# Kernel optimization log

Measured on AMD Instinct MI355X. Metric: run time of the kernel, lower is better.

Reference implementation:

```python
import jax, jax.numpy as jnp
import numpy as np

B, C, H, W = 8, 512, 64, 64
CI = 256  # inter_channels = channel_in // 2
EPS = 1e-5  # BatchNorm eps


def conv1x1(x, w, b):
    # x: (b, c, h, w), w: (o, c), b: (o,)
    return jnp.einsum('bchw,oc->bohw', x, w) + b[None, :, None, None]


def maxpool2(x):
    b, c, h, w = x.shape
    return x.reshape(b, c, h // 2, 2, w // 2, 2).max(axis=(3, 5))


def setup_inputs() -> dict:
    key = jax.random.key(0)
    ks = jax.random.split(key, 13)
    s = 1.0 / np.sqrt(C)
    si = 1.0 / np.sqrt(CI)
    return {
        'x': jax.random.normal(ks[0], (B, C, H, W), dtype=jnp.float32),
        'w_g': jax.random.normal(ks[1], (CI, C), dtype=jnp.float32) * s,
        'b_g': jax.random.normal(ks[2], (CI,), dtype=jnp.float32) * 0.01,
        'w_theta': jax.random.normal(ks[3], (CI, C), dtype=jnp.float32) * s,
        'b_theta': jax.random.normal(ks[4], (CI,), dtype=jnp.float32) * 0.01,
        'w_phi': jax.random.normal(ks[5], (CI, C), dtype=jnp.float32) * s,
        'b_phi': jax.random.normal(ks[6], (CI,), dtype=jnp.float32) * 0.01,
        'w_out': jax.random.normal(ks[7], (C, CI), dtype=jnp.float32) * si,
        'b_out': jax.random.normal(ks[8], (C,), dtype=jnp.float32) * 0.01,
        'bn_gamma': jax.random.normal(ks[9], (C,), dtype=jnp.float32) * 0.1 + 1.0,
        'bn_beta': jax.random.normal(ks[10], (C,), dtype=jnp.float32) * 0.01,
        'bn_mean': jax.random.normal(ks[11], (C,), dtype=jnp.float32) * 0.01,
        'bn_var': jax.random.uniform(ks[12], (C,), dtype=jnp.float32, minval=0.5, maxval=1.5),
    }


def reference(x, w_g, b_g, w_theta, b_theta, w_phi, b_phi,
              w_out, b_out, bn_gamma, bn_beta, bn_mean, bn_var):
    b = x.shape[0]
    # g, phi: 1x1 conv then 2x2 maxpool (sub_sample=True)
    g_x = maxpool2(conv1x1(x, w_g, b_g)).reshape(b, CI, -1)        # (b, ci, M)
    phi_x = maxpool2(conv1x1(x, w_phi, b_phi)).reshape(b, CI, -1)  # (b, ci, M)
    theta_x = conv1x1(x, w_theta, b_theta).reshape(b, CI, -1)      # (b, ci, N)
    # f[b, n, m] = theta^T @ phi  -> softmax over m -> @ g^T
    f = jnp.einsum('bcn,bcm->bnm', theta_x, phi_x)                 # (b, N, M)
    attn = jax.nn.softmax(f, axis=-1)
    y = jnp.einsum('bnm,bcm->bcn', attn, g_x).reshape(b, CI, H, W)
    # W: 1x1 conv + BatchNorm (eval mode, running stats)
    w_y = conv1x1(y, w_out, b_out)
    inv = bn_gamma / jnp.sqrt(bn_var + EPS)
    w_y = w_y * inv[None, :, None, None] + (bn_beta - bn_mean * inv)[None, :, None, None]
    return w_y + x
```

## Files before the change

kernel.cpp:

```cpp
#include <hip/hip_runtime.h>

typedef _Float16 v8h __attribute__((ext_vector_type(8)));
typedef float v4f __attribute__((ext_vector_type(4)));
#define HF _Float16

#define Bn 8
#define Cc 512
#define CI 256
#define HW 4096
#define Mp 1024

__device__ __forceinline__ void gload16(const HF* g, HF* l) {
    __builtin_amdgcn_global_load_lds((const __attribute__((address_space(1))) void*)g,
                                     (__attribute__((address_space(3))) void*)l, 16, 0, 0);
}

__global__ __launch_bounds__(256) void prep_kernel(
    const float* __restrict__ w_g, const float* __restrict__ b_g,
    const float* __restrict__ w_th, const float* __restrict__ b_th,
    const float* __restrict__ w_ph, const float* __restrict__ b_ph,
    const float* __restrict__ w_out, const float* __restrict__ b_out,
    const float* __restrict__ gamma, const float* __restrict__ beta,
    const float* __restrict__ mean, const float* __restrict__ var,
    HF* __restrict__ wall, float* __restrict__ ball,
    HF* __restrict__ wo, float* __restrict__ scale, float* __restrict__ shift)
{
    int idx = blockIdx.x * 256 + threadIdx.x;
    if (idx < 768*512) {
        int o = idx >> 9;
        float v = (o < 256) ? w_th[idx] : (o < 512) ? w_ph[idx - 256*512] : w_g[idx - 512*512];
        wall[idx] = (HF)v;
    }
    if (idx < 512*256) wo[idx] = (HF)w_out[idx];
    if (idx < 768) ball[idx] = (idx < 256) ? b_th[idx] : (idx < 512) ? b_ph[idx-256] : b_g[idx-512];
    if (idx < 512) {
        float inv = gamma[idx] * rsqrtf(var[idx] + 1e-5f);
        scale[idx] = inv;
        shift[idx] = (b_out[idx] - mean[idx]) * inv + beta[idx];
    }
}

__global__ __launch_bounds__(256) void transpose_x_kernel(const float* __restrict__ x, HF* __restrict__ xT)
{
    __shared__ float tile[64][65];
    int b = blockIdx.z;
    int c0 = blockIdx.y * 64, s0 = blockIdx.x * 64;
    int tr = threadIdx.x >> 6, ts = threadIdx.x & 63;
    #pragma unroll
    for (int i = 0; i < 16; ++i) {
        int r = tr + i*4;
        tile[r][ts] = x[((long)(b*Cc) + c0 + r)*HW + s0 + ts];
    }
    __syncthreads();
    #pragma unroll
    for (int i = 0; i < 16; ++i) {
        int r = tr + i*4;
        xT[((long)b*HW + s0 + r)*Cc + c0 + ts] = (HF)tile[ts][r];
    }
}

__global__ __launch_bounds__(256) void transpose_h_kernel(const HF* __restrict__ src, long sSrc,
                                                          HF* __restrict__ dst, long sDst,
                                                          int R, int Cn)
{
    __shared__ HF tile[64][65];
    int b = blockIdx.z;
    int r0 = blockIdx.y * 64, c0 = blockIdx.x * 64;
    const HF* S = src + (long)b * sSrc;
    HF* D = dst + (long)b * sDst;
    int tr = threadIdx.x >> 6, tc = threadIdx.x & 63;
    #pragma unroll
    for (int i = 0; i < 16; ++i) {
        int r = tr + i*4;
        tile[r][tc] = S[(long)(r0 + r)*Cn + c0 + tc];
    }
    __syncthreads();
    #pragma unroll
    for (int i = 0; i < 16; ++i) {
        int r = tr + i*4;
        D[(long)(c0 + r)*R + r0 + tc] = tile[tc][r];
    }
}

__global__ __launch_bounds__(256) void pool_kernel(const HF* __restrict__ src, long sSrc,
                                                   HF* __restrict__ dst, long sDst)
{
    long idx = (long)blockIdx.x * 256 + threadIdx.x;
    int m = idx & 1023;
    long bc = idx >> 10;
    int c = (int)(bc & 255);
    int b = (int)(bc >> 8);
    int h2 = m >> 5, w2 = m & 31;
    const HF* p = src + (long)b*sSrc + (long)c*HW + h2*128 + w2*2;
    float v = fmaxf(fmaxf((float)p[0], (float)p[1]), fmaxf((float)p[64], (float)p[65]));
    dst[(long)b*sDst + (long)c*Mp + m] = (HF)v;
}

template<int EPI>
__global__ __launch_bounds__(256) void gemm_bt_kernel(
    const HF* __restrict__ A, long sA, const HF* __restrict__ B, long sB,
    void* __restrict__ Cv, long sC, int M, int N, int K,
    const float* __restrict__ rowBias,
    const float* __restrict__ rowScale, const float* __restrict__ rowShift,
    const float* __restrict__ Xres, long sX)
{
    __shared__ HF As[128][40];
    __shared__ HF Bs[128][40];
    int b = blockIdx.z;
    int i0 = blockIdx.y * 128;
    int j0 = blockIdx.x * 128;
    const HF* Ab = A + (long)b * sA;
    const HF* Bb = B + (long)b * sB;
    int tid = threadIdx.x;
    int lane = tid & 63, w = tid >> 6;
    int wr = w >> 1, wc = w & 1;
    int lr = lane & 15, lk = (lane >> 4) * 8;

    v4f acc[4][4];
    #pragma unroll
    for (int i = 0; i < 4; ++i)
        #pragma unroll
        for (int j = 0; j < 4; ++j) { v4f z = {0.f,0.f,0.f,0.f}; acc[i][j] = z; }

    for (int k0 = 0; k0 < K; k0 += 32) {
        #pragma unroll
        for (int q = 0; q < 2; ++q) {
            int ch = tid*2 + q;
            int row = ch >> 2;
            int c8 = (ch & 3) * 8;
            const uint4* ga = (const uint4*)(Ab + (long)(i0+row)*K + k0 + c8);
            *(uint4*)(&As[row][c8]) = *ga;
            const uint4* gb = (const uint4*)(Bb + (long)(j0+row)*K + k0 + c8);
            *(uint4*)(&Bs[row][c8]) = *gb;
        }
        __syncthreads();
        v8h af[4], bfr[4];
        #pragma unroll
        for (int mf = 0; mf < 4; ++mf)
            af[mf] = *(const v8h*)(&As[wr*64 + mf*16 + lr][lk]);
        #pragma unroll
        for (int nf = 0; nf < 4; ++nf)
            bfr[nf] = *(const v8h*)(&Bs[wc*64 + nf*16 + lr][lk]);
        #pragma unroll
        for (int mf = 0; mf < 4; ++mf)
            #pragma unroll
            for (int nf = 0; nf < 4; ++nf)
                acc[mf][nf] = __builtin_amdgcn_mfma_f32_16x16x32_f16(af[mf], bfr[nf], acc[mf][nf], 0, 0, 0);
        __syncthreads();
    }

    int rbase = (lane >> 4) * 4;
    #pragma unroll
    for (int mf = 0; mf < 4; ++mf) {
        #pragma unroll
        for (int nf = 0; nf < 4; ++nf) {
            #pragma unroll
            for (int r = 0; r < 4; ++r) {
                int row = i0 + wr*64 + mf*16 + rbase + r;
                int col = j0 + wc*64 + nf*16 + lr;
                float v = acc[mf][nf][r];
                if (EPI == 0) {
                    v += rowBias[row];
                    ((HF*)Cv + (long)b*sC)[(long)row*N + col] = (HF)v;
                } else if (EPI == 1) {
                    ((HF*)Cv + (long)b*sC)[(long)row*N + col] = (HF)v;
                } else {
                    float* Cf = (float*)Cv + (long)b*sC;
                    const float* Xb = Xres + (long)b*sX;
                    long o = (long)row*N + col;
                    Cf[o] = v * rowScale[row] + rowShift[row] + Xb[o];
                }
            }
        }
    }
}

__global__ __launch_bounds__(256) void fused_attn_kernel(
    const HF* __restrict__ Tt,
    const HF* __restrict__ Pt,
    const HF* __restrict__ G,
    HF* __restrict__ Yt)
{
    __shared__ HF P_lds[2][32][256];
    __shared__ HF G_lds[2][256][32];
    __shared__ HF P_buf[4][16][32];

    int b = blockIdx.y;
    int tid = threadIdx.x;
    int lane = tid & 63, w = tid >> 6;
    int lr = lane & 15, lkg = lane >> 4;
    int nbase = blockIdx.x * 64 + w * 16;

    const HF* Tb = Tt + ((long)b*HW + nbase) * CI;
    const HF* Pb = Pt + (long)b*Mp*CI;
    const HF* Gb = G  + (long)b*CI*Mp;

    auto stage = [&](int bsel, int m0) {
        #pragma unroll
        for (int q = 0; q < 4; ++q) {
            int i = w*4 + q;
            int dp = i*512 + lane*8;
            int prow = dp >> 8;
            int pcol = (dp & 255) ^ ((prow & 7) << 3);
            gload16(Pb + (long)(m0 + prow)*CI + pcol, &P_lds[bsel][0][0] + i*512);
            int dg = i*512 + lane*8;
            int grow = dg >> 5;
            int gcol = (dg & 31) ^ ((grow & 3) << 3);
            gload16(Gb + (long)grow*Mp + m0 + gcol, &G_lds[bsel][0][0] + i*512);
        }
    };

    v8h af[8];
    #pragma unroll
    for (int kf = 0; kf < 8; ++kf)
        af[kf] = *(const v8h*)(Tb + (long)lr*CI + kf*32 + lkg*8);

    v4f acc_y[16];
    #pragma unroll
    for (int i = 0; i < 16; ++i) { v4f z = {0.f,0.f,0.f,0.f}; acc_y[i] = z; }
    float mrun[4] = {-1e30f,-1e30f,-1e30f,-1e30f};
    float lrun[4] = {0.f,0.f,0.f,0.f};

    stage(0, 0);
    __syncthreads();

    int cur = 0;
    for (int t = 0; t < 32; ++t) {
        if (t < 31) stage(cur ^ 1, (t+1)*32);

        v4f acc[2];
        #pragma unroll
        for (int nf = 0; nf < 2; ++nf) { v4f z = {0.f,0.f,0.f,0.f}; acc[nf] = z; }
        __builtin_amdgcn_s_setprio(1);
        #pragma unroll
        for (int kf = 0; kf < 8; ++kf) {
            #pragma unroll
            for (int nf = 0; nf < 2; ++nf) {
                int prow = nf*16 + lr;
                v8h bfr = *(const v8h*)(&P_lds[cur][prow][(kf*32 + lkg*8) ^ ((prow & 7) << 3)]);
                acc[nf] = __builtin_amdgcn_mfma_f32_16x16x32_f16(af[kf], bfr, acc[nf], 0, 0, 0);
            }
        }
        __builtin_amdgcn_s_setprio(0);

        #pragma unroll
        for (int r = 0; r < 4; ++r) {
            float cm = fmaxf(acc[0][r], acc[1][r]);
            #pragma unroll
            for (int d = 1; d < 16; d <<= 1) cm = fmaxf(cm, __shfl_xor(cm, d));
            float mold = mrun[r];
            float mnew = fmaxf(mold, cm);
            mrun[r] = mnew;
            if (!__all(cm <= mold)) {
                float alpha = __expf(mold - mnew);
                lrun[r] *= alpha;
                #pragma unroll
                for (int cf = 0; cf < 16; ++cf) acc_y[cf][r] *= alpha;
            }
            int row = lkg*4 + r;
            float rs = 0.f;
            #pragma unroll
            for (int nf = 0; nf < 2; ++nf) {
                float p = __expf(acc[nf][r] - mnew);
                rs += p;
                P_buf[w][row][(nf*16 + lr) ^ ((row & 3) << 3)] = (HF)p;
            }
            #pragma unroll
            for (int d = 1; d < 16; d <<= 1) rs += __shfl_xor(rs, d);
            lrun[r] += rs;
        }

        v8h ap = *(const v8h*)(&P_buf[w][lr][(lkg*8) ^ ((lr & 3) << 3)]);
        __builtin_amdgcn_s_setprio(1);
        #pragma unroll
        for (int cf = 0; cf < 16; ++cf) {
            int grow = cf*16 + lr;
            v8h bg = *(const v8h*)(&G_lds[cur][grow][(lkg*8) ^ ((grow & 3) << 3)]);
            acc_y[cf] = __builtin_amdgcn_mfma_f32_16x16x32_f16(ap, bg, acc_y[cf], 0, 0, 0);
        }
        __builtin_amdgcn_s_setprio(0);

        __syncthreads();
        cur ^= 1;
    }

    HF* Yb = Yt + ((long)b*HW + nbase) * CI;
    #pragma unroll
    for (int r = 0; r < 4; ++r) {
        float inv = 1.f / lrun[r];
        #pragma unroll
        for (int cf = 0; cf < 16; ++cf)
            Yb[(long)(lkg*4 + r)*CI + cf*16 + lr] = (HF)(acc_y[cf][r] * inv);
    }
}

extern "C" void kernel_launch(void* const* d_in, const int* in_sizes, int n_in,
                              void* d_out, int out_size, void* d_ws, size_t ws_size,
                              hipStream_t stream)
{
    const float* x     = (const float*)d_in[0];
    const float* w_g   = (const float*)d_in[1];
    const float* b_g   = (const float*)d_in[2];
    const float* w_th  = (const float*)d_in[3];
    const float* b_th  = (const float*)d_in[4];
    const float* w_ph  = (const float*)d_in[5];
    const float* b_ph  = (const float*)d_in[6];
    const float* w_out = (const float*)d_in[7];
    const float* b_out = (const float*)d_in[8];
    const float* gamma = (const float*)d_in[9];
    const float* beta  = (const float*)d_in[10];
    const float* mean  = (const float*)d_in[11];
    const float* var   = (const float*)d_in[12];
    float* out = (float*)d_out;

    char* ws = (char*)d_ws;
    size_t off = 0;
    auto alloc = [&](size_t bytes) { void* p = ws + off; off += (bytes + 255) & ~(size_t)255; return p; };
    HF*    wall  = (HF*)alloc((size_t)768*512*2);
    float* ball  = (float*)alloc(768*4);
    HF*    wo    = (HF*)alloc((size_t)512*256*2);
    float* scale = (float*)alloc(512*4);
    float* shift = (float*)alloc(512*4);
    HF*    xT    = (HF*)alloc((size_t)Bn*HW*Cc*2);
    HF*    Full  = (HF*)alloc((size_t)Bn*768*HW*2);
    HF*    Tt    = (HF*)alloc((size_t)Bn*HW*CI*2);
    HF*    Pn    = (HF*)alloc((size_t)Bn*CI*Mp*2);
    HF*    Pt    = (HF*)alloc((size_t)Bn*Mp*CI*2);
    HF*    G     = (HF*)alloc((size_t)Bn*CI*Mp*2);
    HF*    Yt    = (HF*)alloc((size_t)Bn*HW*CI*2);

    prep_kernel<<<1536, 256, 0, stream>>>(w_g,b_g,w_th,b_th,w_ph,b_ph,w_out,b_out,gamma,beta,mean,var,
                                          wall, ball, wo, scale, shift);
    transpose_x_kernel<<<dim3(64,8,Bn), 256, 0, stream>>>(x, xT);
    gemm_bt_kernel<0><<<dim3(32,6,Bn), 256, 0, stream>>>(wall, 0, xT, (long)HW*Cc, Full, (long)768*HW,
                                                         768, HW, Cc, ball, nullptr, nullptr, nullptr, 0);
    transpose_h_kernel<<<dim3(64,4,Bn), 256, 0, stream>>>(Full, (long)768*HW, Tt, (long)HW*CI, CI, HW);
    pool_kernel<<<8192, 256, 0, stream>>>(Full + (size_t)256*HW, (long)768*HW, Pn, (long)CI*Mp);
    transpose_h_kernel<<<dim3(16,4,Bn), 256, 0, stream>>>(Pn, (long)CI*Mp, Pt, (long)Mp*CI, CI, Mp);
    pool_kernel<<<8192, 256, 0, stream>>>(Full + (size_t)512*HW, (long)768*HW, G, (long)CI*Mp);
    fused_attn_kernel<<<dim3(64,Bn), 256, 0, stream>>>(Tt, Pt, G, Yt);
    gemm_bt_kernel<2><<<dim3(32,4,Bn), 256, 0, stream>>>(wo, 0, Yt, (long)HW*CI, out, (long)Cc*HW,
                                                         Cc, HW, CI, nullptr, scale, shift, x, (long)Cc*HW);
}
```

Before: 219.6 us.

## Double-buffer GEMM via direct-to-LDS loads and restructure attention LDS layouts

The projection GEMM now uses global_load_lds into double-buffered, k-group-major LDS tiles, so the next K slice loads while the current one runs MFMAs; it also raises MFMA priority. The attention kernel swaps XOR-swizzled LDS layouts for k-group-major layouts and pads P_buf. The softmax row-sum shuffle reduction moves out of the loop to the end, and the kernel gets a two-blocks-per-CU launch bound. The risks are LDS bank conflicts in the new layouts, a divergent rescale branch in place of the wave-uniform check, and register pressure from the occupancy hint.

New measurement: 235.0 us. +7.0%, slower.

```diff
diff --git a/kernel.cpp b/kernel.cpp
--- a/kernel.cpp
+++ b/kernel.cpp
@@ -1,6 +1,7 @@
 #include <hip/hip_runtime.h>
 
 typedef _Float16 v8h __attribute__((ext_vector_type(8)));
+typedef _Float16 v4h __attribute__((ext_vector_type(4)));
 typedef float v4f __attribute__((ext_vector_type(4)));
 #define HF _Float16
 
@@ -10,7 +11,7 @@
 #define HW 4096
 #define Mp 1024
 
-__device__ __forceinline__ void gload16(const HF* g, HF* l) {
+__device__ __forceinline__ void gload16(const void* g, void* l) {
     __builtin_amdgcn_global_load_lds((const __attribute__((address_space(1))) void*)g,
                                      (__attribute__((address_space(3))) void*)l, 16, 0, 0);
 }
@@ -104,8 +105,8 @@
     const float* __restrict__ rowScale, const float* __restrict__ rowShift,
     const float* __restrict__ Xres, long sX)
 {
-    __shared__ HF As[128][40];
-    __shared__ HF Bs[128][40];
+    __shared__ alignas(16) HF As[2][4096];
+    __shared__ alignas(16) HF Bs[2][4096];
     int b = blockIdx.z;
     int i0 = blockIdx.y * 128;
     int j0 = blockIdx.x * 128;
@@ -114,7 +115,17 @@
     int tid = threadIdx.x;
     int lane = tid & 63, w = tid >> 6;
     int wr = w >> 1, wc = w & 1;
-    int lr = lane & 15, lk = (lane >> 4) * 8;
+    int lr = lane & 15, lkg = lane >> 4;
+
+    auto stage = [&](int bsel, int k0) {
+        #pragma unroll
+        for (int q = 0; q < 2; ++q) {
+            int idx = q*256 + tid;
+            int kg = idx >> 7, row = idx & 127;
+            gload16(Ab + (long)(i0+row)*K + k0 + kg*8, As[bsel] + (size_t)idx*8);
+            gload16(Bb + (long)(j0+row)*K + k0 + kg*8, Bs[bsel] + (size_t)idx*8);
+        }
+    };
 
     v4f acc[4][4];
     #pragma unroll
@@ -122,31 +133,27 @@
         #pragma unroll
         for (int j = 0; j < 4; ++j) { v4f z = {0.f,0.f,0.f,0.f}; acc[i][j] = z; }
 
+    stage(0, 0);
+    __syncthreads();
+    int cur = 0;
     for (int k0 = 0; k0 < K; k0 += 32) {
-        #pragma unroll
-        for (int q = 0; q < 2; ++q) {
-            int ch = tid*2 + q;
-            int row = ch >> 2;
-            int c8 = (ch & 3) * 8;
-            const uint4* ga = (const uint4*)(Ab + (long)(i0+row)*K + k0 + c8);
-            *(uint4*)(&As[row][c8]) = *ga;
-            const uint4* gb = (const uint4*)(Bb + (long)(j0+row)*K + k0 + c8);
-            *(uint4*)(&Bs[row][c8]) = *gb;
-        }
-        __syncthreads();
+        if (k0 + 32 < K) stage(cur ^ 1, k0 + 32);
         v8h af[4], bfr[4];
         #pragma unroll
         for (int mf = 0; mf < 4; ++mf)
-            af[mf] = *(const v8h*)(&As[wr*64 + mf*16 + lr][lk]);
+            af[mf] = *(const v8h*)(As[cur] + lkg*1024 + (wr*64 + mf*16 + lr)*8);
         #pragma unroll
         for (int nf = 0; nf < 4; ++nf)
-            bfr[nf] = *(const v8h*)(&Bs[wc*64 + nf*16 + lr][lk]);
+            bfr[nf] = *(const v8h*)(Bs[cur] + lkg*1024 + (wc*64 + nf*16 + lr)*8);
+        __builtin_amdgcn_s_setprio(1);
         #pragma unroll
         for (int mf = 0; mf < 4; ++mf)
             #pragma unroll
             for (int nf = 0; nf < 4; ++nf)
                 acc[mf][nf] = __builtin_amdgcn_mfma_f32_16x16x32_f16(af[mf], bfr[nf], acc[mf][nf], 0, 0, 0);
+        __builtin_amdgcn_s_setprio(0);
         __syncthreads();
+        cur ^= 1;
     }
 
     int rbase = (lane >> 4) * 4;
@@ -161,8 +168,6 @@
                 float v = acc[mf][nf][r];
                 if (EPI == 0) {
                     v += rowBias[row];
-                    ((HF*)Cv + (long)b*sC)[(long)row*N + col] = (HF)v;
-                } else if (EPI == 1) {
                     ((HF*)Cv + (long)b*sC)[(long)row*N + col] = (HF)v;
                 } else {
                     float* Cf = (float*)Cv + (long)b*sC;
@@ -175,15 +180,15 @@
     }
 }
 
-__global__ __launch_bounds__(256) void fused_attn_kernel(
+__global__ __launch_bounds__(256, 2) void fused_attn_kernel(
     const HF* __restrict__ Tt,
     const HF* __restrict__ Pt,
     const HF* __restrict__ G,
     HF* __restrict__ Yt)
 {
-    __shared__ HF P_lds[2][32][256];
-    __shared__ HF G_lds[2][256][32];
-    __shared__ HF P_buf[4][16][32];
+    __shared__ alignas(16) HF P_lds[2][8192];
+    __shared__ alignas(16) HF G_lds[2][8192];
+    __shared__ alignas(16) HF P_buf[4][16][36];
 
     int b = blockIdx.y;
     int tid = threadIdx.x;
@@ -198,15 +203,11 @@
     auto stage = [&](int bsel, int m0) {
         #pragma unroll
         for (int q = 0; q < 4; ++q) {
-            int i = w*4 + q;
-            int dp = i*512 + lane*8;
-            int prow = dp >> 8;
-            int pcol = (dp & 255) ^ ((prow & 7) << 3);
-            gload16(Pb + (long)(m0 + prow)*CI + pcol, &P_lds[bsel][0][0] + i*512);
-            int dg = i*512 + lane*8;
-            int grow = dg >> 5;
-            int gcol = (dg & 31) ^ ((grow & 3) << 3);
-            gload16(Gb + (long)grow*Mp + m0 + gcol, &G_lds[bsel][0][0] + i*512);
+            int idxp = (w*4 + q)*64 + lane;
+            int pkg = idxp >> 5, prow = idxp & 31;
+            gload16(Pb + (long)(m0 + prow)*CI + pkg*8, P_lds[bsel] + (size_t)idxp*8);
+            int grow = q*64 + lane;
+            gload16(Gb + (long)grow*Mp + m0 + w*8, G_lds[bsel] + ((size_t)w*256 + grow)*8);
         }
     };
 
@@ -219,7 +220,7 @@
     #pragma unroll
     for (int i = 0; i < 16; ++i) { v4f z = {0.f,0.f,0.f,0.f}; acc_y[i] = z; }
     float mrun[4] = {-1e30f,-1e30f,-1e30f,-1e30f};
-    float lrun[4] = {0.f,0.f,0.f,0.f};
+    float lsum[4] = {0.f,0.f,0.f,0.f};
 
     stage(0, 0);
     __syncthreads();
@@ -236,8 +237,7 @@
         for (int kf = 0; kf < 8; ++kf) {
             #pragma unroll
             for (int nf = 0; nf < 2; ++nf) {
-                int prow = nf*16 + lr;
-                v8h bfr = *(const v8h*)(&P_lds[cur][prow][(kf*32 + lkg*8) ^ ((prow & 7) << 3)]);
+                v8h bfr = *(const v8h*)(P_lds[cur] + (kf*4 + lkg)*256 + (nf*16 + lr)*8);
                 acc[nf] = __builtin_amdgcn_mfma_f32_16x16x32_f16(af[kf], bfr, acc[nf], 0, 0, 0);
             }
         }
@@ -248,34 +248,29 @@
             float cm = fmaxf(acc[0][r], acc[1][r]);
             #pragma unroll
             for (int d = 1; d < 16; d <<= 1) cm = fmaxf(cm, __shfl_xor(cm, d));
-            float mold = mrun[r];
-            float mnew = fmaxf(mold, cm);
-            mrun[r] = mnew;
-            if (!__all(cm <= mold)) {
-                float alpha = __expf(mold - mnew);
-                lrun[r] *= alpha;
+            if (cm > mrun[r]) {
+                float alpha = __expf(mrun[r] - cm);
+                mrun[r] = cm;
+                lsum[r] *= alpha;
                 #pragma unroll
                 for (int cf = 0; cf < 16; ++cf) acc_y[cf][r] *= alpha;
             }
             int row = lkg*4 + r;
-            float rs = 0.f;
             #pragma unroll
             for (int nf = 0; nf < 2; ++nf) {
-                float p = __expf(acc[nf][r] - mnew);
-                rs += p;
-                P_buf[w][row][(nf*16 + lr) ^ ((row & 3) << 3)] = (HF)p;
+                float p = __expf(acc[nf][r] - mrun[r]);
+                lsum[r] += p;
+                P_buf[w][row][nf*16 + lr] = (HF)p;
             }
-            #pragma unroll
-            for (int d = 1; d < 16; d <<= 1) rs += __shfl_xor(rs, d);
-            lrun[r] += rs;
-        }
-
-        v8h ap = *(const v8h*)(&P_buf[w][lr][(lkg*8) ^ ((lr & 3) << 3)]);
+        }
+
+        v4h plo = *(const v4h*)(&P_buf[w][lr][lkg*8]);
+        v4h phi = *(const v4h*)(&P_buf[w][lr][lkg*8 + 4]);
+        v8h ap = __builtin_shufflevector(plo, phi, 0,1,2,3,4,5,6,7);
         __builtin_amdgcn_s_setprio(1);
         #pragma unroll
         for (int cf = 0; cf < 16; ++cf) {
-            int grow = cf*16 + lr;
-            v8h bg = *(const v8h*)(&G_lds[cur][grow][(lkg*8) ^ ((grow & 3) << 3)]);
+            v8h bg = *(const v8h*)(G_lds[cur] + lkg*2048 + (cf*16 + lr)*8);
             acc_y[cf] = __builtin_amdgcn_mfma_f32_16x16x32_f16(ap, bg, acc_y[cf], 0, 0, 0);
         }
         __builtin_amdgcn_s_setprio(0);
@@ -287,7 +282,10 @@
     HF* Yb = Yt + ((long)b*HW + nbase) * CI;
     #pragma unroll
     for (int r = 0; r < 4; ++r) {
-        float inv = 1.f / lrun[r];
+        float s = lsum[r];
+        #pragma unroll
+        for (int d = 1; d < 16; d <<= 1) s += __shfl_xor(s, d);
+        float inv = 1.f / s;
         #pragma unroll
         for (int cf = 0; cf < 16; ++cf)
             Yb[(long)(lkg*4 + r)*CI + cf*16 + lr] = (HF)(acc_y[cf][r] * inv);
```
